# Performance work log

Hardware: AMD Instinct MI355X
Metric: run time of the kernel (lower is better)

Reference implementation:

```python
import jax, jax.numpy as jnp
import numpy as np

# Directable[TL_table[i]] for i = 0..7: (dx, dy) with dx=horizontal shift, dy=vertical shift
# dx=+1 -> shift right (zero-fill col 0), dx=-1 -> shift left; dy=+1 -> shift down, dy=-1 -> shift up.
DIRS = [(1, 1), (0, 1), (-1, 1), (1, 0), (-1, 0), (1, -1), (0, -1), (-1, -1)]


def _shift(img, dx, dy):
    # img: [B, H, W]; zero-padded shift equivalent to bmm with the sparse translation matrices
    if dx == 1:
        img = jnp.pad(img[..., :-1], ((0, 0), (0, 0), (1, 0)))
    elif dx == -1:
        img = jnp.pad(img[..., 1:], ((0, 0), (0, 0), (0, 1)))
    if dy == 1:
        img = jnp.pad(img[:, :-1, :], ((0, 0), (1, 0), (0, 0)))
    elif dy == -1:
        img = jnp.pad(img[:, 1:, :], ((0, 0), (0, 1), (0, 0)))
    return img


def _bce(p, t):
    # torch F.binary_cross_entropy clamps log terms at -100
    logp = jnp.maximum(jnp.log(p), -100.0)
    log1mp = jnp.maximum(jnp.log(1.0 - p), -100.0)
    return -jnp.mean(t * logp + (1.0 - t) * log1mp)


def setup_inputs() -> dict:
    key = jax.random.key(0)
    k1, k2, k3 = jax.random.split(key, 3)
    B, C, H, W = 16, 8, 512, 512
    c_map = jax.random.normal(k1, (B, C, H, W), dtype=jnp.float32)
    target = jax.random.randint(k2, (B, 1, H, W), 0, 2, dtype=jnp.int32)
    con_target = jax.random.randint(k3, (B, C, H, W), 0, 2, dtype=jnp.int32)
    return {"c_map": c_map, "target": target, "con_target": con_target}


def reference(c_map, target, con_target):
    target = target.astype(jnp.float32)        # [B,1,H,W]
    con_target = con_target.astype(jnp.float32)  # [B,8,H,W]

    p = jax.nn.sigmoid(c_map)  # [B,8,H,W]

    # Bilateral voting: shifted[i] = shift(p[:, 7-i]) in direction DIRS[i]
    shifted = jnp.stack(
        [_shift(p[:, 7 - i], dx, dy) for i, (dx, dy) in enumerate(DIRS)], axis=1
    )  # [B,8,H,W]
    vote_out = p * shifted                       # [B,8,H,W] (== bimap.squeeze(1))
    final_pred = jnp.max(vote_out, axis=1, keepdims=True)  # [B,1,H,W]

    # dice loss (sums over dims (1,2) of the 4D tensors, as in the original)
    smooth = 0.001
    i_sum = jnp.sum(target, axis=(1, 2))
    j_sum = jnp.sum(final_pred, axis=(1, 2))
    inter = jnp.sum(target * final_pred, axis=(1, 2))
    loss_dice = jnp.mean(1.0 - (2.0 * inter + smooth) / (i_sum + j_sum + smooth))

    # edge (decouple) loss
    sum_conn = jnp.sum(con_target, axis=1)  # [B,H,W]
    edge = ((sum_conn < 8) & (sum_conn > 0)).astype(p.dtype)
    pred_min = jnp.min(vote_out, axis=1) * edge
    decouple_loss = _bce(pred_min, jnp.zeros_like(pred_min))

    bce_loss = _bce(final_pred, target)
    conmap_l = _bce(p, con_target)
    bimap_l = _bce(vote_out, con_target)

    return 0.8 * conmap_l + decouple_loss + 0.2 * bimap_l + bce_loss + loss_dice
```

## Files before the change

### kernel.cpp

```cpp
#include <hip/hip_runtime.h>

namespace {
constexpr int Bn = 16, Hn = 512, Wn = 512;
constexpr int HW  = Hn * Wn;
constexpr int CHW = 8 * HW;
constexpr int NCOL = Bn * Wn;
constexpr int WALK = 4;
constexpr int ROWSB = 2 * WALK;
constexpr int GX   = Hn / ROWSB;
constexpr int NBLK = GX * Bn;
constexpr int FBLK = 32;

__device__ __forceinline__ float frcp(float x) { return __builtin_amdgcn_rcpf(x); }
__device__ __forceinline__ float fsig(float x) { return frcp(1.f + __expf(-x)); }
}


__global__ __launch_bounds__(256) void bicon_main(
    const float* __restrict__ c_map,
    const int*   __restrict__ target,
    const int*   __restrict__ con_target,
    float* __restrict__ col_i, float* __restrict__ col_j, float* __restrict__ col_x,
    double* __restrict__ bscal)
{
    const int tid  = threadIdx.x;
    const int lane = tid & 63;
    const int wv   = tid >> 6;
    const int half = wv & 1;
    const int rg   = wv >> 1;
    const int b    = blockIdx.y;
    const int hstart = blockIdx.x * ROWSB + rg * WALK;
    const int wq   = half * 256 + lane * 4;

    const float* cm = c_map      + (size_t)b * CHW;
    const int*   ct = con_target + (size_t)b * CHW;
    const int*   tg = target     + (size_t)b * HW;

    float s_con = 0.f, s_bi = 0.f, s_bce = 0.f, s_dec = 0.f;
    float ci[4] = {0, 0, 0, 0}, cj[4] = {0, 0, 0, 0}, cx[4] = {0, 0, 0, 0};

    auto sig4 = [&](const float4& v, float s[4]) {
        s[0] = fsig(v.x); s[1] = fsig(v.y); s[2] = fsig(v.z); s[3] = fsig(v.w);
    };

    float C0[4], C1[4], C2[4];
    float P5[4], P6[4], P7[4];
    {
        const int pb = hstart * Wn + wq;
        sig4(*(const float4*)(cm + 0 * HW + pb), C0);
        sig4(*(const float4*)(cm + 1 * HW + pb), C1);
        sig4(*(const float4*)(cm + 2 * HW + pb), C2);
    }
    if (hstart > 0) {
        const int pb = (hstart - 1) * Wn + wq;
        sig4(*(const float4*)(cm + 5 * HW + pb), P5);
        sig4(*(const float4*)(cm + 6 * HW + pb), P6);
        sig4(*(const float4*)(cm + 7 * HW + pb), P7);
    } else {
#pragma unroll
        for (int k = 0; k < 4; ++k) { P5[k] = 0.f; P6[k] = 0.f; P7[k] = 0.f; }
    }

    const bool edR = (wq + 4 == Wn);
    const bool edL = (wq == 0);

    int h = hstart;
#pragma unroll 1
    for (int r = 0; r < WALK; ++r, ++h) {
        const int  base  = h * Wn + wq;
        const bool hasDn = (h + 1 < Hn);
        const bool hasUp = (h > 0);

        const float4 xf0 = *(const float4*)(cm + 0 * HW + base + Wn);
        const float4 xf1 = *(const float4*)(cm + 1 * HW + base + Wn);
        const float4 xf2 = *(const float4*)(cm + 2 * HW + base + Wn);
        const float bx0 = cm[0 * HW + base + Wn + 4];
        const float bx2 = cm[2 * HW + base + Wn - 1];
        const float bx3 = cm[3 * HW + base + 4];
        const float bx4 = cm[4 * HW + base - 1];
        const float bx5 = cm[5 * HW + base - Wn + 4];
        const float bx7 = cm[7 * HW + base - Wn - 1];
        const int4 t4  = *(const int4*)(tg + base);

        unsigned lo = 0u;
#pragma unroll
        for (int c = 0; c < 8; ++c) {
            const int4 u = *(const int4*)(ct + c * HW + base);
            lo |= ((unsigned)u.x << c)        | ((unsigned)u.y << (8 + c)) |
                  ((unsigned)u.z << (16 + c)) | ((unsigned)u.w << (24 + c));
        }

#pragma unroll
        for (int k = 0; k < 4; ++k) {
            s_con += fmaxf(__logf(((lo >> (8 * k + 0)) & 1u) ? C0[k] : 1.f - C0[k]), -100.f);
            s_con += fmaxf(__logf(((lo >> (8 * k + 1)) & 1u) ? C1[k] : 1.f - C1[k]), -100.f);
            s_con += fmaxf(__logf(((lo >> (8 * k + 2)) & 1u) ? C2[k] : 1.f - C2[k]), -100.f);
        }

        float c3[4], c4[4], c5[4], c6[4], c7[4];
        auto sigcon = [&](int c, float s[4]) {
            const float4 v = *(const float4*)(cm + c * HW + base);
            const float xs[4] = {v.x, v.y, v.z, v.w};
#pragma unroll
            for (int k = 0; k < 4; ++k) {
                const float e = __expf(-xs[k]);
                const float d = 1.f + e;
                s[k] = frcp(d);
                const float logd = __logf(d);
                s_con += fmaxf(((lo >> (8 * k + c)) & 1u) ? -logd : (-xs[k] - logd),
                               -100.f);
            }
        };
        sigcon(3, c3); sigcon(4, c4); sigcon(5, c5); sigcon(6, c6); sigcon(7, c7);

        float F0[4], F1[4], F2[4];
        sig4(xf0, F0); sig4(xf1, F1); sig4(xf2, F2);

        const float s0b = fsig(bx0), s2b = fsig(bx2), s3b = fsig(bx3);
        const float s4b = fsig(bx4), s5b = fsig(bx5), s7b = fsig(bx7);

        float n0[4], n1[4], n2[4], n3[4], n4[4], n5[4], n6[4], n7[4];
#pragma unroll
        for (int k = 0; k < 3; ++k) {
            n0[k] = F0[k + 1]; n3[k] = c3[k + 1]; n5[k] = P5[k + 1];
            n2[k + 1] = F2[k]; n4[k + 1] = c4[k]; n7[k + 1] = P7[k];
        }
        n0[3] = edR ? 0.f : s0b;  n3[3] = edR ? 0.f : s3b;  n5[3] = edR ? 0.f : s5b;
        n2[0] = edL ? 0.f : s2b;  n4[0] = edL ? 0.f : s4b;  n7[0] = edL ? 0.f : s7b;
#pragma unroll
        for (int k = 0; k < 4; ++k) {
            n1[k] = hasDn ? F1[k] : 0.f;
            n6[k] = hasUp ? P6[k] : 0.f;
            if (!hasDn) { n0[k] = 0.f; n2[k] = 0.f; }
            if (!hasUp) { n5[k] = 0.f; n7[k] = 0.f; }
        }

        float vmax[4] = {0.f, 0.f, 0.f, 0.f}, vmin[4] = {2.f, 2.f, 2.f, 2.f};
        auto vote = [&](int i, const float p[4], const float n[4]) {
#pragma unroll
            for (int k = 0; k < 4; ++k) {
                const float v = p[k] * n[k];
                vmax[k] = fmaxf(vmax[k], v);
                vmin[k] = fminf(vmin[k], v);
                s_bi += fmaxf(__logf(((lo >> (8 * k + i)) & 1u) ? v : 1.f - v),
                              -100.f);
            }
        };
        vote(0, C0, n7); vote(1, C1, n6); vote(2, C2, n5); vote(3, c3, n4);
        vote(4, c4, n3); vote(5, c5, n2); vote(6, c6, n1); vote(7, c7, n0);

        const int tk[4] = {t4.x, t4.y, t4.z, t4.w};
#pragma unroll
        for (int k = 0; k < 4; ++k) {
            const float fm = vmax[k];
            s_bce += fmaxf(__logf(tk[k] ? fm : 1.f - fm), -100.f);
            const int sc = __popc((int)((lo >> (8 * k)) & 0xffu));
            s_dec += (sc > 0 && sc < 8)
                         ? fmaxf(__logf(1.f - vmin[k]), -100.f) : 0.f;
            ci[k] += (float)tk[k];
            cj[k] += fm;
            cx[k] += tk[k] ? fm : 0.f;
        }

#pragma unroll
        for (int k = 0; k < 4; ++k) {
            C0[k] = F0[k]; C1[k] = F1[k]; C2[k] = F2[k];
            P5[k] = c5[k]; P6[k] = c6[k]; P7[k] = c7[k];
        }
    }

    __shared__ float cred[3][4][256];
#pragma unroll
    for (int k = 0; k < 4; ++k) {
        cred[0][wv][(lane << 2) + k] = ci[k];
        cred[1][wv][(lane << 2) + k] = cj[k];
        cred[2][wv][(lane << 2) + k] = cx[k];
    }

#pragma unroll
    for (int off = 32; off > 0; off >>= 1) {
        s_con += __shfl_down(s_con, off);
        s_bi  += __shfl_down(s_bi,  off);
        s_bce += __shfl_down(s_bce, off);
        s_dec += __shfl_down(s_dec, off);
    }
    __shared__ float wred[4][4];
    if (lane == 0) {
        wred[wv][0] = s_con; wred[wv][1] = s_bi;
        wred[wv][2] = s_bce; wred[wv][3] = s_dec;
    }
    __syncthreads();

#pragma unroll
    for (int j = tid; j < 512; j += 256) {
        const int hj = j >> 8, cidx = j & 255;
        const float a0 = cred[0][hj][cidx] + cred[0][hj + 2][cidx];
        const float a1 = cred[1][hj][cidx] + cred[1][hj + 2][cidx];
        const float a2 = cred[2][hj][cidx] + cred[2][hj + 2][cidx];
        atomicAdd(&col_i[b * Wn + j], a0);
        atomicAdd(&col_j[b * Wn + j], a1);
        atomicAdd(&col_x[b * Wn + j], a2);
    }
    if (tid < 4) {
        bscal[((size_t)blockIdx.y * GX + blockIdx.x) * 4 + tid] =
            (double)(wred[0][tid] + wred[1][tid] + wred[2][tid] + wred[3][tid]);
    }
}

__global__ __launch_bounds__(256) void bicon_finish(
    const float* __restrict__ col_i,
    const float* __restrict__ col_j,
    const float* __restrict__ col_x,
    const double* __restrict__ bscal,
    float* __restrict__ out)
{
    const int tid = threadIdx.x;
    const int col = blockIdx.x * 256 + tid;

    double part;
    {
        const float fi = col_i[col], fj = col_j[col], fx = col_x[col];
        part = (1.0 - (2.0 * (double)fx + 0.001) /
                      ((double)fi + (double)fj + 0.001)) / 8192.0;
    }
    if (tid < 32) {
        const int s = blockIdx.x * 32 + tid;
        const double c0 = bscal[s * 4 + 0], c1 = bscal[s * 4 + 1];
        const double c2 = bscal[s * 4 + 2], c3 = bscal[s * 4 + 3];
        part += -0.8 * c0 / 33554432.0 - 0.2 * c1 / 33554432.0
                - c2 / 4194304.0 - c3 / 4194304.0;
    }
#pragma unroll
    for (int off = 32; off > 0; off >>= 1) part += __shfl_down(part, off);
    __shared__ double red[4];
    if ((tid & 63) == 0) red[tid >> 6] = part;
    __syncthreads();
    if (tid == 0) atomicAdd(out, (float)(red[0] + red[1] + red[2] + red[3]));
}

extern "C" void kernel_launch(void* const* d_in, const int* in_sizes, int n_in,
                              void* d_out, int out_size, void* d_ws, size_t ws_size,
                              hipStream_t stream) {
    const float* c_map      = (const float*)d_in[0];
    const int*   target     = (const int*)d_in[1];
    const int*   con_target = (const int*)d_in[2];
    float* out = (float*)d_out;

    char* ws = (char*)d_ws;
    float*  col_i = (float*)ws;
    float*  col_j = col_i + NCOL;
    float*  col_x = col_j + NCOL;
    double* bscal = (double*)(ws + 3 * NCOL * sizeof(float));

    hipMemsetAsync(d_ws, 0, 3 * NCOL * sizeof(float), stream);
    hipMemsetAsync(d_out, 0, sizeof(float), stream);

    dim3 grid(GX, Bn);
    dim3 block(256);
    bicon_main<<<grid, block, 0, stream>>>(c_map, target, con_target,
                                           col_i, col_j, col_x, bscal);
    bicon_finish<<<FBLK, 256, 0, stream>>>(col_i, col_j, col_x, bscal, out);
}
```

Measured before the change: 308.1 us.

## Batch BCE logs into products with base-2 exp/log and halve rows per block

Replaces per-element natural log/exp with hardware exp2/log2 intrinsics and folds the ln2 scaling into the final reduction. The conmap and bimap BCE terms now multiply several probabilities and take one log2 per group instead of one log per channel. Exact zeros are tracked separately so the -100 clamp still applies. WALK drops from 4 to 2, which doubles the block count and the partial sums the finish kernel reads. The product trick skips the per-term clamp for tiny nonzero values and risks underflow when several small factors are multiplied.

```diff
diff --git a/kernel.cpp b/kernel.cpp
--- a/kernel.cpp
+++ b/kernel.cpp
@@ -5,14 +5,26 @@
 constexpr int HW  = Hn * Wn;
 constexpr int CHW = 8 * HW;
 constexpr int NCOL = Bn * Wn;
-constexpr int WALK = 4;
-constexpr int ROWSB = 2 * WALK;
-constexpr int GX   = Hn / ROWSB;
+constexpr int WALK = 2;
+constexpr int GX   = Hn / (2 * WALK);
 constexpr int NBLK = GX * Bn;
 constexpr int FBLK = 32;
 
+constexpr float L2E  = 1.4426950408889634f;
+constexpr float LN2  = 0.6931471805599453f;
+constexpr float CLMP = -144.26950408889634f;
+
 __device__ __forceinline__ float frcp(float x) { return __builtin_amdgcn_rcpf(x); }
-__device__ __forceinline__ float fsig(float x) { return frcp(1.f + __expf(-x)); }
+#if __has_builtin(__builtin_amdgcn_exp2f)
+__device__ __forceinline__ float fexp2(float x) { return __builtin_amdgcn_exp2f(x); }
+#else
+__device__ __forceinline__ float fexp2(float x) { return exp2f(x); }
+#endif
+#if __has_builtin(__builtin_amdgcn_logf)
+__device__ __forceinline__ float flog2(float x) { return __builtin_amdgcn_logf(x); }
+#else
+__device__ __forceinline__ float flog2(float x) { return log2f(x); }
+#endif
 }
 
 
@@ -29,7 +41,7 @@
     const int half = wv & 1;
     const int rg   = wv >> 1;
     const int b    = blockIdx.y;
-    const int hstart = blockIdx.x * ROWSB + rg * WALK;
+    const int hstart = blockIdx.x * (2 * WALK) + rg * WALK;
     const int wq   = half * 256 + lane * 4;
 
     const float* cm = c_map      + (size_t)b * CHW;
@@ -40,11 +52,13 @@
     float ci[4] = {0, 0, 0, 0}, cj[4] = {0, 0, 0, 0}, cx[4] = {0, 0, 0, 0};
 
     auto sig4 = [&](const float4& v, float s[4]) {
-        s[0] = fsig(v.x); s[1] = fsig(v.y); s[2] = fsig(v.z); s[3] = fsig(v.w);
+        s[0] = frcp(1.f + fexp2(-v.x * L2E));
+        s[1] = frcp(1.f + fexp2(-v.y * L2E));
+        s[2] = frcp(1.f + fexp2(-v.z * L2E));
+        s[3] = frcp(1.f + fexp2(-v.w * L2E));
     };
 
-    float C0[4], C1[4], C2[4];
-    float P5[4], P6[4], P7[4];
+    float C0[4], C1[4], C2[4], P5[4], P6[4], P7[4];
     {
         const int pb = hstart * Wn + wq;
         sig4(*(const float4*)(cm + 0 * HW + pb), C0);
@@ -71,6 +85,11 @@
         const bool hasDn = (h + 1 < Hn);
         const bool hasUp = (h > 0);
 
+        const float4 xa3 = *(const float4*)(cm + 3 * HW + base);
+        const float4 xa4 = *(const float4*)(cm + 4 * HW + base);
+        const float4 xa5 = *(const float4*)(cm + 5 * HW + base);
+        const float4 xa6 = *(const float4*)(cm + 6 * HW + base);
+        const float4 xa7 = *(const float4*)(cm + 7 * HW + base);
         const float4 xf0 = *(const float4*)(cm + 0 * HW + base + Wn);
         const float4 xf1 = *(const float4*)(cm + 1 * HW + base + Wn);
         const float4 xf2 = *(const float4*)(cm + 2 * HW + base + Wn);
@@ -80,7 +99,7 @@
         const float bx4 = cm[4 * HW + base - 1];
         const float bx5 = cm[5 * HW + base - Wn + 4];
         const float bx7 = cm[7 * HW + base - Wn - 1];
-        const int4 t4  = *(const int4*)(tg + base);
+        const int4  t4  = *(const int4*)(tg + base);
 
         unsigned lo = 0u;
 #pragma unroll
@@ -90,34 +109,40 @@
                   ((unsigned)u.z << (16 + c)) | ((unsigned)u.w << (24 + c));
         }
 
-#pragma unroll
-        for (int k = 0; k < 4; ++k) {
-            s_con += fmaxf(__logf(((lo >> (8 * k + 0)) & 1u) ? C0[k] : 1.f - C0[k]), -100.f);
-            s_con += fmaxf(__logf(((lo >> (8 * k + 1)) & 1u) ? C1[k] : 1.f - C1[k]), -100.f);
-            s_con += fmaxf(__logf(((lo >> (8 * k + 2)) & 1u) ? C2[k] : 1.f - C2[k]), -100.f);
-        }
-
+        float dp[4] = {1.f, 1.f, 1.f, 1.f};
+        float ys[4] = {0.f, 0.f, 0.f, 0.f};
         float c3[4], c4[4], c5[4], c6[4], c7[4];
-        auto sigcon = [&](int c, float s[4]) {
-            const float4 v = *(const float4*)(cm + c * HW + base);
+        auto fresh = [&](int c, const float4& v, float s[4]) {
             const float xs[4] = {v.x, v.y, v.z, v.w};
 #pragma unroll
             for (int k = 0; k < 4; ++k) {
-                const float e = __expf(-xs[k]);
+                const float y = xs[k] * L2E;
+                const float e = fexp2(-y);
                 const float d = 1.f + e;
                 s[k] = frcp(d);
-                const float logd = __logf(d);
-                s_con += fmaxf(((lo >> (8 * k + c)) & 1u) ? -logd : (-xs[k] - logd),
-                               -100.f);
+                dp[k] *= d;
+                ys[k] += ((lo >> (8 * k + c)) & 1u) ? 0.f : y;
             }
         };
-        sigcon(3, c3); sigcon(4, c4); sigcon(5, c5); sigcon(6, c6); sigcon(7, c7);
+        fresh(3, xa3, c3); fresh(4, xa4, c4); fresh(5, xa5, c5);
+        fresh(6, xa6, c6); fresh(7, xa7, c7);
+
+#pragma unroll
+        for (int k = 0; k < 4; ++k) {
+            const float q0 = ((lo >> (8 * k + 0)) & 1u) ? C0[k] : 1.f - C0[k];
+            const float q1 = ((lo >> (8 * k + 1)) & 1u) ? C1[k] : 1.f - C1[k];
+            const float q2 = ((lo >> (8 * k + 2)) & 1u) ? C2[k] : 1.f - C2[k];
+            s_con += flog2(q0 * q1 * q2) - flog2(dp[k]) - ys[k];
+        }
 
         float F0[4], F1[4], F2[4];
         sig4(xf0, F0); sig4(xf1, F1); sig4(xf2, F2);
-
-        const float s0b = fsig(bx0), s2b = fsig(bx2), s3b = fsig(bx3);
-        const float s4b = fsig(bx4), s5b = fsig(bx5), s7b = fsig(bx7);
+        const float s0b = frcp(1.f + fexp2(-bx0 * L2E));
+        const float s2b = frcp(1.f + fexp2(-bx2 * L2E));
+        const float s3b = frcp(1.f + fexp2(-bx3 * L2E));
+        const float s4b = frcp(1.f + fexp2(-bx4 * L2E));
+        const float s5b = frcp(1.f + fexp2(-bx5 * L2E));
+        const float s7b = frcp(1.f + fexp2(-bx7 * L2E));
 
         float n0[4], n1[4], n2[4], n3[4], n4[4], n5[4], n6[4], n7[4];
 #pragma unroll
@@ -136,27 +161,36 @@
         }
 
         float vmax[4] = {0.f, 0.f, 0.f, 0.f}, vmin[4] = {2.f, 2.f, 2.f, 2.f};
+        float pr[4]   = {1.f, 1.f, 1.f, 1.f};
+        float zc[4]   = {0.f, 0.f, 0.f, 0.f};
         auto vote = [&](int i, const float p[4], const float n[4]) {
 #pragma unroll
             for (int k = 0; k < 4; ++k) {
                 const float v = p[k] * n[k];
                 vmax[k] = fmaxf(vmax[k], v);
                 vmin[k] = fminf(vmin[k], v);
-                s_bi += fmaxf(__logf(((lo >> (8 * k + i)) & 1u) ? v : 1.f - v),
-                              -100.f);
+                const bool bit = (lo >> (8 * k + i)) & 1u;
+                const bool z   = bit && (v == 0.f);
+                float sel = bit ? v : 1.f - v;
+                sel = z ? 1.f : sel;
+                zc[k] += z ? 1.f : 0.f;
+                pr[k] *= sel;
             }
         };
         vote(0, C0, n7); vote(1, C1, n6); vote(2, C2, n5); vote(3, c3, n4);
+#pragma unroll
+        for (int k = 0; k < 4; ++k) { s_bi += flog2(pr[k]); pr[k] = 1.f; }
         vote(4, c4, n3); vote(5, c5, n2); vote(6, c6, n1); vote(7, c7, n0);
+#pragma unroll
+        for (int k = 0; k < 4; ++k) { s_bi += flog2(pr[k]) + CLMP * zc[k]; }
 
         const int tk[4] = {t4.x, t4.y, t4.z, t4.w};
 #pragma unroll
         for (int k = 0; k < 4; ++k) {
             const float fm = vmax[k];
-            s_bce += fmaxf(__logf(tk[k] ? fm : 1.f - fm), -100.f);
+            s_bce += fmaxf(flog2(tk[k] ? fm : 1.f - fm), CLMP);
             const int sc = __popc((int)((lo >> (8 * k)) & 0xffu));
-            s_dec += (sc > 0 && sc < 8)
-                         ? fmaxf(__logf(1.f - vmin[k]), -100.f) : 0.f;
+            s_dec += (sc > 0 && sc < 8) ? fmaxf(flog2(1.f - vmin[k]), CLMP) : 0.f;
             ci[k] += (float)tk[k];
             cj[k] += fm;
             cx[k] += tk[k] ? fm : 0.f;
@@ -186,20 +220,17 @@
     }
     __shared__ float wred[4][4];
     if (lane == 0) {
-        wred[wv][0] = s_con; wred[wv][1] = s_bi;
-        wred[wv][2] = s_bce; wred[wv][3] = s_dec;
+        wred[wv][0] = s_con * LN2; wred[wv][1] = s_bi * LN2;
+        wred[wv][2] = s_bce * LN2; wred[wv][3] = s_dec * LN2;
     }
     __syncthreads();
 
 #pragma unroll
     for (int j = tid; j < 512; j += 256) {
         const int hj = j >> 8, cidx = j & 255;
-        const float a0 = cred[0][hj][cidx] + cred[0][hj + 2][cidx];
-        const float a1 = cred[1][hj][cidx] + cred[1][hj + 2][cidx];
-        const float a2 = cred[2][hj][cidx] + cred[2][hj + 2][cidx];
-        atomicAdd(&col_i[b * Wn + j], a0);
-        atomicAdd(&col_j[b * Wn + j], a1);
-        atomicAdd(&col_x[b * Wn + j], a2);
+        atomicAdd(&col_i[b * Wn + j], cred[0][hj][cidx] + cred[0][hj + 2][cidx]);
+        atomicAdd(&col_j[b * Wn + j], cred[1][hj][cidx] + cred[1][hj + 2][cidx]);
+        atomicAdd(&col_x[b * Wn + j], cred[2][hj][cidx] + cred[2][hj + 2][cidx]);
     }
     if (tid < 4) {
         bscal[((size_t)blockIdx.y * GX + blockIdx.x) * 4 + tid] =
@@ -223,8 +254,8 @@
         part = (1.0 - (2.0 * (double)fx + 0.001) /
                       ((double)fi + (double)fj + 0.001)) / 8192.0;
     }
-    if (tid < 32) {
-        const int s = blockIdx.x * 32 + tid;
+    if (tid < 64) {
+        const int s = blockIdx.x * 64 + tid;
         const double c0 = bscal[s * 4 + 0], c1 = bscal[s * 4 + 1];
         const double c2 = bscal[s * 4 + 2], c3 = bscal[s * 4 + 3];
         part += -0.8 * c0 / 33554432.0 - 0.2 * c1 / 33554432.0
```

Result: no change. 303.1 us (-1.6%).
